# Performance work log

Measured on AMD Instinct MI355X. Metric: run time of the kernel, lower is better.

The kernel has to match this reference:

```python
import jax, jax.numpy as jnp
import numpy as np

LENS = 0.4
DECAY = 0.2
THRESH = 0.2
LOG_SIG_MIN, LOG_SIG_MAX = -20.0, 2.0

# Surrogate-gradient spike: forward is heaviside, backward is rectangular window |x|<lens
@jax.custom_vjp
def act_fun(x):
    return (x > 0.0).astype(x.dtype)

def _act_fwd(x):
    return act_fun(x), x

def _act_bwd(x, g):
    return (g * (jnp.abs(x) < LENS).astype(g.dtype),)

act_fun.defvjp(_act_fwd, _act_bwd)


def _xavier(k, shape):
    fan_out, fan_in = shape
    lim = float(np.sqrt(6.0 / (fan_in + fan_out)))
    return jax.random.uniform(k, shape, jnp.float32, -lim, lim)


def setup_inputs() -> dict:
    key = jax.random.key(0)
    ks = jax.random.split(key, 9)
    B, IN, H, A = 4096, 512, 2048, 32
    return {
        "state": jax.random.normal(ks[0], (B, 5, IN), jnp.float32),
        "W_lif": _xavier(ks[1], (H, IN)), "b_lif": jnp.zeros((H,), jnp.float32),
        "W11": _xavier(ks[2], (H, H)), "b11": jnp.zeros((H,), jnp.float32),
        "W12": _xavier(ks[3], (H, H)), "b12": jnp.zeros((H,), jnp.float32),
        "W21": _xavier(ks[4], (H, H)), "b21": jnp.zeros((H,), jnp.float32),
        "W22": _xavier(ks[5], (H, H)), "b22": jnp.zeros((H,), jnp.float32),
        "Wm": _xavier(ks[6], (A, H)), "bm": jnp.zeros((A,), jnp.float32),
        "Wls": _xavier(ks[7], (A, H)), "bls": jnp.zeros((A,), jnp.float32),
    }


def reference(state, W_lif, b_lif, W11, b11, W12, b12, W21, b21, W22, b22, Wm, bm, Wls, bls):
    x_seq = jnp.repeat(state, 3, axis=1)
    # precompute fc(x) for all steps in one GEMM: [B,15,H]
    fc = jnp.einsum('bti,hi->bth', x_seq, W_lif) + b_lif
    B, T, H = fc.shape

    def step(carry, fc_t):
        mem, spike = carry
        mem1 = mem * DECAY * (1.0 - spike) + fc_t
        spike1 = act_fun(mem1 - THRESH)
        return (mem1, spike1), spike1

    init = (jnp.zeros((B, H), fc.dtype), jnp.zeros((B, H), fc.dtype))
    _, spikes = jax.lax.scan(step, init, jnp.swapaxes(fc, 0, 1))  # [T,B,H]
    x = jnp.mean(spikes, axis=0)  # [B,H]

    x1 = jax.nn.relu(x @ W11.T + b11)
    x1 = jax.nn.relu(x1 @ W12.T + b12)
    mean = x1 @ Wm.T + bm

    x2 = jax.nn.relu(x @ W21.T + b21)
    x2 = jax.nn.relu(x2 @ W22.T + b22)
    log_std = jnp.clip(x2 @ Wls.T + bls, LOG_SIG_MIN, LOG_SIG_MAX)
    return mean, log_std
```

## Files before the change

### kernel.cpp

```cpp
#include <hip/hip_runtime.h>
#include <hip/hip_bf16.h>


typedef _Float16 f16;
using f32x4 = __attribute__((ext_vector_type(4))) float;
using f16x8 = __attribute__((ext_vector_type(8))) f16;

#define MFMA16(a, b, c) __builtin_amdgcn_mfma_f32_16x16x32_f16((a), (b), (c), 0, 0, 0)
#define VMW6()  asm volatile("s_waitcnt vmcnt(6)" ::: "memory")
#define VMW4()  asm volatile("s_waitcnt vmcnt(4)" ::: "memory")
#define VMW0()  asm volatile("s_waitcnt vmcnt(0)" ::: "memory")
#define LGKM0() asm volatile("s_waitcnt lgkmcnt(0)" ::: "memory")
#define BARRIER() __builtin_amdgcn_s_barrier()
#define SCHED0() __builtin_amdgcn_sched_barrier(0)

__device__ __forceinline__ void gload16(const void* g, void* l) {
  __builtin_amdgcn_global_load_lds(
      (const __attribute__((address_space(1))) unsigned int*)g,
      (__attribute__((address_space(3))) unsigned int*)l, 16, 0, 0);
}

__device__ __forceinline__ void cvt8(const float4& a, const float4& b, f16* dst) {
  f16x8 d;
  d[0] = (f16)a.x; d[1] = (f16)a.y; d[2] = (f16)a.z; d[3] = (f16)a.w;
  d[4] = (f16)b.x; d[5] = (f16)b.y; d[6] = (f16)b.z; d[7] = (f16)b.w;
  *(f16x8*)dst = d;
}

__global__ __launch_bounds__(256) void cvtall_kernel(
    const float* __restrict__ state, const float* __restrict__ wlif,
    const float* __restrict__ w11, const float* __restrict__ w21,
    const float* __restrict__ w12, const float* __restrict__ w22,
    const float* __restrict__ wm, const float* __restrict__ wls,
    f16* __restrict__ s16, f16* __restrict__ wl16, f16* __restrict__ w4,
    f16* __restrict__ wmh, f16* __restrict__ wlsh)
{
  int i = blockIdx.x * 256 + threadIdx.x;
  const float* src; f16* dst; int k, ks;
  if (i < 1310720)        { src = state; dst = s16;  k = i;           ks = k; }
  else if (i < 1441792)   { src = wlif;  dst = wl16; k = i - 1310720; ks = k; }
  else if (i < 3538944) {
    int j = i - 1441792; int w = j >> 19;
    src = (w == 0) ? w11 : (w == 1) ? w21 : (w == 2) ? w12 : w22;
    dst = w4; k = j; ks = j & 524287;
  }
  else if (i < 3547136)   { src = wm;  dst = wmh;  k = i - 3538944; ks = k; }
  else if (i < 3555328)   { src = wls; dst = wlsh; k = i - 3547136; ks = k; }
  else return;
  const float4* s4 = (const float4*)src;
  float4 a = s4[(size_t)ks * 2], b = s4[(size_t)ks * 2 + 1];
  cvt8(a, b, dst + (size_t)k * 8);
}

__global__ __launch_bounds__(512, 1) void lif256_kernel(
    const f16* __restrict__ S,
    const f16* __restrict__ W,
    const float* __restrict__ bl,
    f16* __restrict__ X)
{
  __shared__ alignas(16) f16 lds[73728];

  const int tid = threadIdx.x, wid = tid >> 6, lane = tid & 63;
  const int wg = ((int)blockIdx.x % 8) * 32 + (int)blockIdx.x / 8;
  const int bn = wg & 15, bm = wg >> 4;
  const int b0 = bm * 256, h0 = bn * 128;
  const int wr0 = (wid >> 1) * 64, wc0 = (wid & 1) * 64;
  const int fr = lane & 15, fq = lane >> 4;
  const int sr = tid >> 3, scb = (tid & 7) * 16;

  f32x4 acc[4][4] = {};
  float mem[4][4][4] = {};
  unsigned pcnt[4][4] = {};

  char* Lb = (char*)&lds[0];
  const int xsw = (fr & 7) << 4;
  const int x0 = (fq * 16) ^ xsw;
  const int x1 = (64 + fq * 16) ^ xsw;
  char* const pA0 = Lb + (wr0 + fr) * 128 + x0;
  char* const pA1 = Lb + (wr0 + fr) * 128 + x1;
  char* const pB0 = Lb + 98304 + (wc0 + fr) * 128 + x0;
  char* const pB1 = Lb + 98304 + (wc0 + fr) * 128 + x1;

  const f16* sBase[4]; const f16* wBase[2];
#pragma unroll
  for (int l = 0; l < 4; ++l) {
    const int row = l * 64 + sr;
    const int c2 = scb ^ ((row & 7) << 4);
    sBase[l] = S + (size_t)(b0 + row) * 2560 + (c2 >> 1);
  }
#pragma unroll
  for (int l = 0; l < 2; ++l) {
    const int row = l * 64 + sr;
    const int c2 = scb ^ ((row & 7) << 4);
    wBase[l] = W + (size_t)(h0 + row) * 512 + (c2 >> 1);
  }

  auto STAGE = [&](int soA, int soB, int g) {
    const int koff = (g >> 3) * 512 + (g & 7) * 64;
    const int kw = (g & 7) * 64;
#pragma unroll
    for (int l = 0; l < 4; ++l)
      gload16(sBase[l] + koff, Lb + soA + l * 8192 + tid * 16);
#pragma unroll
    for (int l = 0; l < 2; ++l)
      gload16(wBase[l] + kw, Lb + 98304 + soB + l * 8192 + tid * 16);
  };

  const float bias[4] = { bl[h0 + wc0 + fr],      bl[h0 + wc0 + 16 + fr],
                          bl[h0 + wc0 + 32 + fr], bl[h0 + wc0 + 48 + fr] };

  auto LIFBURST = [&]() {
#pragma unroll
    for (int mf = 0; mf < 4; ++mf)
#pragma unroll
      for (int nf = 0; nf < 4; ++nf) {
        unsigned pc = pcnt[mf][nf];
#pragma unroll
        for (int r = 0; r < 4; ++r) {
          const float fc = acc[mf][nf][r] + bias[nf];
          float m = mem[mf][nf][r];
          const unsigned inc = 1u << (8 * r);
#pragma unroll
          for (int j = 0; j < 3; ++j) {
            m = ((m > 0.2f) ? 0.f : m * 0.2f) + fc;
            pc += (m > 0.2f) ? inc : 0u;
          }
          mem[mf][nf][r] = m;
        }
        pcnt[mf][nf] = pc;
        acc[mf][nf] = f32x4{0.f, 0.f, 0.f, 0.f};
      }
  };

  STAGE(0, 0, 0);
  STAGE(32768, 16384, 1);
  VMW6();
  BARRIER();
  SCHED0();

  int soA = 0, soB = 0;
  int soStA = 65536, soStB = 32768;
  for (int g = 0; g < 40; ++g) {
    if (g + 2 < 40) STAGE(soStA, soStB, g + 2);
    SCHED0();

    if ((g & 7) == 0 && g > 0) LIFBURST();

    f16x8 b[4][2], a[4][2];
#pragma unroll
    for (int nf = 0; nf < 4; ++nf) {
      b[nf][0] = *(const f16x8*)(pB0 + soB + nf * 2048);
      b[nf][1] = *(const f16x8*)(pB1 + soB + nf * 2048);
    }
#pragma unroll
    for (int mf = 0; mf < 4; ++mf) {
      a[mf][0] = *(const f16x8*)(pA0 + soA + mf * 2048);
      a[mf][1] = *(const f16x8*)(pA1 + soA + mf * 2048);
    }

    __builtin_amdgcn_s_setprio(1);
#pragma unroll
    for (int mf = 0; mf < 4; ++mf)
#pragma unroll
      for (int nf = 0; nf < 4; ++nf) {
        acc[mf][nf] = MFMA16(a[mf][0], b[nf][0], acc[mf][nf]);
        acc[mf][nf] = MFMA16(a[mf][1], b[nf][1], acc[mf][nf]);
      }
    __builtin_amdgcn_s_setprio(0);

    LGKM0();
    if (g + 2 < 40)      { VMW6(); }
    else if (g + 1 < 40) { VMW0(); }
    BARRIER();
    SCHED0();

    soA   = (soA   == 65536) ? 0 : soA   + 32768;
    soB   = (soB   == 32768) ? 0 : soB   + 16384;
    soStA = (soStA == 65536) ? 0 : soStA + 32768;
    soStB = (soStB == 32768) ? 0 : soStB + 16384;
  }

  LIFBURST();

#pragma unroll
  for (int nf = 0; nf < 4; ++nf) {
    const int col = h0 + wc0 + nf * 16 + fr;
#pragma unroll
    for (int mf = 0; mf < 4; ++mf) {
      const int row0 = b0 + wr0 + mf * 16 + fq * 4;
#pragma unroll
      for (int r = 0; r < 4; ++r) {
        const float c = (float)((pcnt[mf][nf] >> (8 * r)) & 255u);
        X[(size_t)(row0 + r) * 2048 + col] = (f16)(c / 15.0f);
      }
    }
  }
}

__global__ __launch_bounds__(512, 2) void trunk256_kernel(
    const f16* __restrict__ A0, const f16* __restrict__ A1, int lda,
    const f16* __restrict__ W0, const f16* __restrict__ W1,
    const float* __restrict__ bb0, const float* __restrict__ bb1,
    f16* __restrict__ C0, f16* __restrict__ C1, int ldc,
    int nbm, int nbn_half, int K)
{
  __shared__ alignas(16) f16 lds[4][256 * 64];

  const int tid = threadIdx.x, wid = tid >> 6, lane = tid & 63;
  const int nwg = nbm * nbn_half * 2, q8 = nwg / 8;
  const int wg = ((int)blockIdx.x % 8) * q8 + (int)blockIdx.x / 8;
  const int bmi = wg % nbm, t = wg / nbm;
  const int half = (t >= nbn_half);
  const f16* Ap = half ? A1 : A0;
  const f16* Wp = half ? W1 : W0;
  const float* bias = half ? bb1 : bb0;
  f16* C = half ? C1 : C0;
  const int bm0 = bmi * 256;
  const int bn0 = (half ? t - nbn_half : t) * 256;

  const int wr0 = (wid >> 2) * 128, wc0 = (wid & 3) * 64;
  const int fr = lane & 15, fq = lane >> 4;
  const int sr = tid >> 3, scb = (tid & 7) * 16;

  f32x4 acc[8][4] = {};

  char* Lb = (char*)&lds[0][0];
  const int xsw = (fr & 7) << 4;
  const int x0 = (fq * 16) ^ xsw;
  const int x1 = (64 + fq * 16) ^ xsw;
  char* const pA0 = Lb + (wr0 + fr) * 128 + x0;
  char* const pA1 = Lb + (wr0 + fr) * 128 + x1;
  char* const pB0 = Lb + 65536 + (wc0 + fr) * 128 + x0;
  char* const pB1 = Lb + 65536 + (wc0 + fr) * 128 + x1;

  const f16* aBase[4]; const f16* wBase[4];
#pragma unroll
  for (int l = 0; l < 4; ++l) {
    const int row = l * 64 + sr;
    const int c2 = scb ^ ((row & 7) << 4);
    aBase[l] = Ap + (size_t)(bm0 + row) * lda + (c2 >> 1);
    wBase[l] = Wp + (size_t)(bn0 + row) * K + (c2 >> 1);
  }

  auto STG_A = [&](int bufoff, int h, int kt) {
    const int koff = kt * 64;
#pragma unroll
    for (int l = 2 * h; l < 2 * h + 2; ++l)
      gload16(aBase[l] + koff, Lb + bufoff + l * 8192 + tid * 16);
  };
  auto STG_B = [&](int bufoff, int h, int kt) {
    const int koff = kt * 64;
#pragma unroll
    for (int l = 2 * h; l < 2 * h + 2; ++l)
      gload16(wBase[l] + koff, Lb + 65536 + bufoff + l * 8192 + tid * 16);
  };

  auto QUAD = [&](int mbase, f16x8 (&b)[4][2], f16x8 (&a)[2][2]) {
    __builtin_amdgcn_s_setprio(1);
#pragma unroll
    for (int nf = 0; nf < 4; ++nf) {
      acc[mbase][nf]     = MFMA16(a[0][0], b[nf][0], acc[mbase][nf]);
      acc[mbase][nf]     = MFMA16(a[0][1], b[nf][1], acc[mbase][nf]);
      acc[mbase + 1][nf] = MFMA16(a[1][0], b[nf][0], acc[mbase + 1][nf]);
      acc[mbase + 1][nf] = MFMA16(a[1][1], b[nf][1], acc[mbase + 1][nf]);
    }
    __builtin_amdgcn_s_setprio(0);
  };

  STG_B(0, 0, 0); STG_B(0, 1, 0);
  STG_A(0, 0, 0); STG_A(0, 1, 0);
  STG_B(32768, 0, 1); STG_B(32768, 1, 1);
  VMW0();
  BARRIER();
  SCHED0();

  f16x8 b[4][2], a[2][2];
  for (int i = 0; i < 16; ++i) {
    const int t1 = 2 * i + 1, u = 2 * i + 2, v = 2 * i + 3;
    const bool su = (u < 32), sv = (v < 32);

#pragma unroll
    for (int nf = 0; nf < 4; ++nf) {
      b[nf][0] = *(const f16x8*)(pB0 + nf * 2048);
      b[nf][1] = *(const f16x8*)(pB1 + nf * 2048);
    }
#pragma unroll
    for (int j = 0; j < 2; ++j) {
      a[j][0] = *(const f16x8*)(pA0 + j * 2048);
      a[j][1] = *(const f16x8*)(pA1 + j * 2048);
    }
    STG_A(32768, 0, t1);
    LGKM0(); BARRIER(); SCHED0();
    QUAD(0, b, a);

#pragma unroll
    for (int j = 0; j < 2; ++j) {
      a[j][0] = *(const f16x8*)(pA0 + (2 + j) * 2048);
      a[j][1] = *(const f16x8*)(pA1 + (2 + j) * 2048);
    }
    STG_A(32768, 1, t1);
    LGKM0(); BARRIER(); SCHED0();
    QUAD(2, b, a);

#pragma unroll
    for (int j = 0; j < 2; ++j) {
      a[j][0] = *(const f16x8*)(pA0 + (4 + j) * 2048);
      a[j][1] = *(const f16x8*)(pA1 + (4 + j) * 2048);
    }
    if (su) STG_B(0, 0, u);
    LGKM0(); BARRIER(); SCHED0();
    QUAD(4, b, a);

#pragma unroll
    for (int j = 0; j < 2; ++j) {
      a[j][0] = *(const f16x8*)(pA0 + (6 + j) * 2048);
      a[j][1] = *(const f16x8*)(pA1 + (6 + j) * 2048);
    }
    if (su) STG_B(0, 1, u);
    LGKM0();
    if (su) { VMW4(); } else { VMW0(); }
    BARRIER(); SCHED0();
    QUAD(6, b, a);

#pragma unroll
    for (int nf = 0; nf < 4; ++nf) {
      b[nf][0] = *(const f16x8*)(pB0 + 32768 + nf * 2048);
      b[nf][1] = *(const f16x8*)(pB1 + 32768 + nf * 2048);
    }
#pragma unroll
    for (int j = 0; j < 2; ++j) {
      a[j][0] = *(const f16x8*)(pA0 + 32768 + j * 2048);
      a[j][1] = *(const f16x8*)(pA1 + 32768 + j * 2048);
    }
    if (su) STG_A(0, 0, u);
    LGKM0(); BARRIER(); SCHED0();
    QUAD(0, b, a);

#pragma unroll
    for (int j = 0; j < 2; ++j) {
      a[j][0] = *(const f16x8*)(pA0 + 32768 + (2 + j) * 2048);
      a[j][1] = *(const f16x8*)(pA1 + 32768 + (2 + j) * 2048);
    }
    if (su) STG_A(0, 1, u);
    LGKM0(); BARRIER(); SCHED0();
    QUAD(2, b, a);

#pragma unroll
    for (int j = 0; j < 2; ++j) {
      a[j][0] = *(const f16x8*)(pA0 + 32768 + (4 + j) * 2048);
      a[j][1] = *(const f16x8*)(pA1 + 32768 + (4 + j) * 2048);
    }
    if (sv) STG_B(32768, 0, v);
    LGKM0(); BARRIER(); SCHED0();
    QUAD(4, b, a);

#pragma unroll
    for (int j = 0; j < 2; ++j) {
      a[j][0] = *(const f16x8*)(pA0 + 32768 + (6 + j) * 2048);
      a[j][1] = *(const f16x8*)(pA1 + 32768 + (6 + j) * 2048);
    }
    if (sv) STG_B(32768, 1, v);
    LGKM0();
    if (sv) { VMW4(); } else { VMW0(); }
    BARRIER(); SCHED0();
    QUAD(6, b, a);
  }

#pragma unroll
  for (int nf = 0; nf < 4; ++nf) {
    const int col = bn0 + wc0 + nf * 16 + fr;
    const float bv = bias[col];
#pragma unroll
    for (int m = 0; m < 8; ++m) {
      const int row0 = bm0 + wr0 + m * 16 + fq * 4;
#pragma unroll
      for (int r = 0; r < 4; ++r) {
        float v = fmaxf(acc[m][nf][r] + bv, 0.f);
        C[(size_t)(row0 + r) * ldc + col] = (f16)v;
      }
    }
  }
}

__global__ __launch_bounds__(256) void head_kernel(
    const f16* __restrict__ H1, const f16* __restrict__ H2,
    const f16* __restrict__ Wm, const float* __restrict__ bm,
    const f16* __restrict__ Wls, const float* __restrict__ bls,
    float* __restrict__ OUT, int M, int K)
{
  const int tid = threadIdx.x, wid = tid >> 6, lane = tid & 63;
  const int m0 = blockIdx.x * 64 + wid * 16;
  const int kb = (lane >> 4) * 8, fr = lane & 15, fq = lane >> 4;

  f32x4 a1[2] = {}, a2[2] = {};
  for (int k0 = 0; k0 < K; k0 += 32) {
    f16x8 f1 = *(const f16x8*)&H1[(size_t)(m0 + fr) * K + k0 + kb];
    f16x8 f2 = *(const f16x8*)&H2[(size_t)(m0 + fr) * K + k0 + kb];
#pragma unroll
    for (int n = 0; n < 2; ++n) {
      f16x8 wm = *(const f16x8*)&Wm[(size_t)(n * 16 + fr) * K + k0 + kb];
      f16x8 wl = *(const f16x8*)&Wls[(size_t)(n * 16 + fr) * K + k0 + kb];
      a1[n] = MFMA16(f1, wm, a1[n]);
      a2[n] = MFMA16(f2, wl, a2[n]);
    }
  }

#pragma unroll
  for (int n = 0; n < 2; ++n) {
    const int col = n * 16 + fr;
    const float bvm = bm[col];
    const float bvl = bls[col];
#pragma unroll
    for (int r = 0; r < 4; ++r) {
      const int row = m0 + fq * 4 + r;
      OUT[(size_t)row * 32 + col] = a1[n][r] + bvm;
      float lv = a2[n][r] + bvl;
      OUT[(size_t)M * 32 + (size_t)row * 32 + col] = fminf(fmaxf(lv, -20.f), 2.f);
    }
  }
}

extern "C" void kernel_launch(void* const* d_in, const int* in_sizes, int n_in,
                              void* d_out, int out_size, void* d_ws, size_t ws_size,
                              hipStream_t stream) {
  const float* state = (const float*)d_in[0];
  const float* W_lif = (const float*)d_in[1];
  const float* b_lif = (const float*)d_in[2];
  const float* W11   = (const float*)d_in[3];
  const float* b11   = (const float*)d_in[4];
  const float* W12   = (const float*)d_in[5];
  const float* b12   = (const float*)d_in[6];
  const float* W21   = (const float*)d_in[7];
  const float* b21   = (const float*)d_in[8];
  const float* W22   = (const float*)d_in[9];
  const float* b22   = (const float*)d_in[10];
  const float* Wm    = (const float*)d_in[11];
  const float* bm    = (const float*)d_in[12];
  const float* Wls   = (const float*)d_in[13];
  const float* bls   = (const float*)d_in[14];
  float* out = (float*)d_out;

  const int B = 4096, H = 2048;
  char* ws = (char*)d_ws;
  f16* x    = (f16*)(ws);
  f16* s16  = (f16*)(ws + 16777216);
  f16* h1   = (f16*)(ws + 16777216);
  f16* h2   = (f16*)(ws + 33554432);
  f16* wl16 = (f16*)(ws + 37748736);
  f16* w4   = (f16*)(ws + 50331648);
  f16* w11h = (f16*)(ws + 50331648);
  f16* w21h = (f16*)(ws + 58720256);
  f16* h22  = (f16*)(ws + 50331648);
  f16* w12h = (f16*)(ws + 67108864);
  f16* w22h = (f16*)(ws + 75497472);
  f16* wmh  = (f16*)(ws + 83886080);
  f16* wlsh = (f16*)(ws + 84017152);
  f16* h12  = x;

  cvtall_kernel<<<13888, 256, 0, stream>>>(
      state, W_lif, W11, W21, W12, W22, Wm, Wls,
      s16, wl16, w4, wmh, wlsh);

  lif256_kernel<<<256, 512, 0, stream>>>(s16, wl16, b_lif, x);

  trunk256_kernel<<<256, 512, 0, stream>>>(x, x, H, w11h, w21h, b11, b21,
                                           h1, h2, H, 16, 8, H);
  trunk256_kernel<<<256, 512, 0, stream>>>(h1, h2, H, w12h, w22h, b12, b22,
                                           h12, h22, H, 16, 8, H);

  head_kernel<<<B / 64, 256, 0, stream>>>(h12, h22, wmh, bm, wlsh, bls, out, B, H);
}
```

Measured before the change: 255.2 us.

## Fuse fp32-to-fp16 state conversion into the LIF GEMM load path

Drops the state tensor from the bulk conversion pre-pass. The LIF kernel now reads fp32 state straight into registers, converts it to fp16 and writes it to swizzled LDS after the MFMA block. Weights still use direct global-to-LDS loads. This removes a full write and re-read of a roughly 20 MB fp16 copy of the state. The cost is twice the global bytes for the state reads inside the GEMM, plus conversion work and register pressure in its main loop.

```diff
diff --git a/kernel.cpp b/kernel.cpp
--- a/kernel.cpp
+++ b/kernel.cpp
@@ -7,7 +7,6 @@
 using f16x8 = __attribute__((ext_vector_type(8))) f16;
 
 #define MFMA16(a, b, c) __builtin_amdgcn_mfma_f32_16x16x32_f16((a), (b), (c), 0, 0, 0)
-#define VMW6()  asm volatile("s_waitcnt vmcnt(6)" ::: "memory")
 #define VMW4()  asm volatile("s_waitcnt vmcnt(4)" ::: "memory")
 #define VMW0()  asm volatile("s_waitcnt vmcnt(0)" ::: "memory")
 #define LGKM0() asm volatile("s_waitcnt lgkmcnt(0)" ::: "memory")
@@ -28,24 +27,23 @@
 }
 
 __global__ __launch_bounds__(256) void cvtall_kernel(
-    const float* __restrict__ state, const float* __restrict__ wlif,
+    const float* __restrict__ wlif,
     const float* __restrict__ w11, const float* __restrict__ w21,
     const float* __restrict__ w12, const float* __restrict__ w22,
     const float* __restrict__ wm, const float* __restrict__ wls,
-    f16* __restrict__ s16, f16* __restrict__ wl16, f16* __restrict__ w4,
+    f16* __restrict__ wl16, f16* __restrict__ w4,
     f16* __restrict__ wmh, f16* __restrict__ wlsh)
 {
   int i = blockIdx.x * 256 + threadIdx.x;
   const float* src; f16* dst; int k, ks;
-  if (i < 1310720)        { src = state; dst = s16;  k = i;           ks = k; }
-  else if (i < 1441792)   { src = wlif;  dst = wl16; k = i - 1310720; ks = k; }
-  else if (i < 3538944) {
-    int j = i - 1441792; int w = j >> 19;
+  if (i < 131072)         { src = wlif; dst = wl16; k = i; ks = k; }
+  else if (i < 2228224) {
+    int j = i - 131072; int w = j >> 19;
     src = (w == 0) ? w11 : (w == 1) ? w21 : (w == 2) ? w12 : w22;
     dst = w4; k = j; ks = j & 524287;
   }
-  else if (i < 3547136)   { src = wm;  dst = wmh;  k = i - 3538944; ks = k; }
-  else if (i < 3555328)   { src = wls; dst = wlsh; k = i - 3547136; ks = k; }
+  else if (i < 2236416)   { src = wm;  dst = wmh;  k = i - 2228224; ks = k; }
+  else if (i < 2244608)   { src = wls; dst = wlsh; k = i - 2236416; ks = k; }
   else return;
   const float4* s4 = (const float4*)src;
   float4 a = s4[(size_t)ks * 2], b = s4[(size_t)ks * 2 + 1];
@@ -53,7 +51,7 @@
 }
 
 __global__ __launch_bounds__(512, 1) void lif256_kernel(
-    const f16* __restrict__ S,
+    const float* __restrict__ Sf,
     const f16* __restrict__ W,
     const float* __restrict__ bl,
     f16* __restrict__ X)
@@ -81,12 +79,12 @@
   char* const pB0 = Lb + 98304 + (wc0 + fr) * 128 + x0;
   char* const pB1 = Lb + 98304 + (wc0 + fr) * 128 + x1;
 
-  const f16* sBase[4]; const f16* wBase[2];
+  const float* sBase[4]; const f16* wBase[2];
 #pragma unroll
   for (int l = 0; l < 4; ++l) {
     const int row = l * 64 + sr;
     const int c2 = scb ^ ((row & 7) << 4);
-    sBase[l] = S + (size_t)(b0 + row) * 2560 + (c2 >> 1);
+    sBase[l] = Sf + (size_t)(b0 + row) * 2560 + (c2 >> 1);
   }
 #pragma unroll
   for (int l = 0; l < 2; ++l) {
@@ -94,17 +92,6 @@
     const int c2 = scb ^ ((row & 7) << 4);
     wBase[l] = W + (size_t)(h0 + row) * 512 + (c2 >> 1);
   }
-
-  auto STAGE = [&](int soA, int soB, int g) {
-    const int koff = (g >> 3) * 512 + (g & 7) * 64;
-    const int kw = (g & 7) * 64;
-#pragma unroll
-    for (int l = 0; l < 4; ++l)
-      gload16(sBase[l] + koff, Lb + soA + l * 8192 + tid * 16);
-#pragma unroll
-    for (int l = 0; l < 2; ++l)
-      gload16(wBase[l] + kw, Lb + 98304 + soB + l * 8192 + tid * 16);
-  };
 
   const float bias[4] = { bl[h0 + wc0 + fr],      bl[h0 + wc0 + 16 + fr],
                           bl[h0 + wc0 + 32 + fr], bl[h0 + wc0 + 48 + fr] };
@@ -132,16 +119,52 @@
       }
   };
 
-  STAGE(0, 0, 0);
-  STAGE(32768, 16384, 1);
-  VMW6();
+  float4 av[4][2];
+
+#pragma unroll
+  for (int l = 0; l < 4; ++l) {
+    av[l][0] = *(const float4*)(sBase[l] + 0);
+    av[l][1] = *(const float4*)(sBase[l] + 4);
+  }
+#pragma unroll
+  for (int l = 0; l < 2; ++l)
+    gload16(wBase[l] + 0, Lb + 98304 + l * 8192 + tid * 16);
+#pragma unroll
+  for (int l = 0; l < 4; ++l)
+    cvt8(av[l][0], av[l][1], (f16*)(Lb + l * 8192 + tid * 16));
+#pragma unroll
+  for (int l = 0; l < 4; ++l) {
+    av[l][0] = *(const float4*)(sBase[l] + 64);
+    av[l][1] = *(const float4*)(sBase[l] + 68);
+  }
+#pragma unroll
+  for (int l = 0; l < 2; ++l)
+    gload16(wBase[l] + 64, Lb + 98304 + 16384 + l * 8192 + tid * 16);
+#pragma unroll
+  for (int l = 0; l < 4; ++l)
+    cvt8(av[l][0], av[l][1], (f16*)(Lb + 32768 + l * 8192 + tid * 16));
+  LGKM0();
+  VMW0();
   BARRIER();
   SCHED0();
 
   int soA = 0, soB = 0;
   int soStA = 65536, soStB = 32768;
   for (int g = 0; g < 40; ++g) {
-    if (g + 2 < 40) STAGE(soStA, soStB, g + 2);
+    const bool st = (g + 2 < 40);
+    if (st) {
+      const int g2 = g + 2;
+      const int koff = (g2 >> 3) * 512 + (g2 & 7) * 64;
+      const int kw = (g2 & 7) * 64;
+#pragma unroll
+      for (int l = 0; l < 4; ++l) {
+        av[l][0] = *(const float4*)(sBase[l] + koff);
+        av[l][1] = *(const float4*)(sBase[l] + koff + 4);
+      }
+#pragma unroll
+      for (int l = 0; l < 2; ++l)
+        gload16(wBase[l] + kw, Lb + 98304 + soStB + l * 8192 + tid * 16);
+    }
     SCHED0();
 
     if ((g & 7) == 0 && g > 0) LIFBURST();
@@ -168,9 +191,14 @@
       }
     __builtin_amdgcn_s_setprio(0);
 
+    SCHED0();
+    if (st) {
+#pragma unroll
+      for (int l = 0; l < 4; ++l)
+        cvt8(av[l][0], av[l][1], (f16*)(Lb + soStA + l * 8192 + tid * 16));
+    }
     LGKM0();
-    if (g + 2 < 40)      { VMW6(); }
-    else if (g + 1 < 40) { VMW0(); }
+    if (!st && g + 1 < 40) { VMW0(); }
     BARRIER();
     SCHED0();
 
@@ -443,7 +471,6 @@
   const int B = 4096, H = 2048;
   char* ws = (char*)d_ws;
   f16* x    = (f16*)(ws);
-  f16* s16  = (f16*)(ws + 16777216);
   f16* h1   = (f16*)(ws + 16777216);
   f16* h2   = (f16*)(ws + 33554432);
   f16* wl16 = (f16*)(ws + 37748736);
@@ -457,11 +484,11 @@
   f16* wlsh = (f16*)(ws + 84017152);
   f16* h12  = x;
 
-  cvtall_kernel<<<13888, 256, 0, stream>>>(
-      state, W_lif, W11, W21, W12, W22, Wm, Wls,
-      s16, wl16, w4, wmh, wlsh);
-
-  lif256_kernel<<<256, 512, 0, stream>>>(s16, wl16, b_lif, x);
+  cvtall_kernel<<<8768, 256, 0, stream>>>(
+      W_lif, W11, W21, W12, W22, Wm, Wls,
+      wl16, w4, wmh, wlsh);
+
+  lif256_kernel<<<256, 512, 0, stream>>>(state, wl16, b_lif, x);
 
   trunk256_kernel<<<256, 512, 0, stream>>>(x, x, H, w11h, w21h, b11, b21,
                                            h1, h2, H, 16, 8, H);
```

Result: slower. 310.2 us (+21.5%).
